# Optimization experiments

Measured on AMD Instinct MI355X. Metric: run time of the kernel, lower is better.

## Reference

```python
import jax, jax.numpy as jnp
import numpy as np

N_NODES = 50000
N_EDGES = 1600000
IN_C = 64
OUT_C = 64
N_CLASSES = 45


def setup_inputs() -> dict:
    key = jax.random.key(0)
    ks = jax.random.split(key, 12)

    def lin(k, i, o):
        return jax.random.normal(k, (i, o), jnp.float32) / np.float32(np.sqrt(i))

    return dict(
        x=jax.random.normal(ks[0], (N_NODES, IN_C), jnp.float32),
        edge_index=jax.random.randint(ks[1], (2, N_EDGES), 0, N_NODES, dtype=jnp.int32),
        W_z=lin(ks[2], IN_C, OUT_C), b_z=jnp.zeros((OUT_C,), jnp.float32),
        Wl_z=lin(ks[3], 2 * OUT_C, OUT_C), bl_z=jnp.zeros((OUT_C,), jnp.float32),
        W_r=lin(ks[4], IN_C, OUT_C), b_r=jnp.zeros((OUT_C,), jnp.float32),
        Wl_r=lin(ks[5], 2 * OUT_C, OUT_C), bl_r=jnp.zeros((OUT_C,), jnp.float32),
        W_h=lin(ks[6], IN_C, OUT_C), b_h=jnp.zeros((OUT_C,), jnp.float32),
        Wl_h=lin(ks[7], 2 * OUT_C, OUT_C), bl_h=jnp.zeros((OUT_C,), jnp.float32),
        W_out=lin(ks[8], OUT_C, N_CLASSES), b_out=jnp.zeros((N_CLASSES,), jnp.float32),
    )


def _gcn(x, W, b, src, dst, dinv):
    # GCNConv with improved self-loops (fill value 2.0):
    # out = D^{-1/2} (A + 2I) D^{-1/2} X W + b, with deg = in_degree + 2
    xw = x @ W                                   # [N, OUT_C]
    norm = dinv[src] * dinv[dst]                 # [E]
    agg = jax.ops.segment_sum(norm[:, None] * xw[src], dst, num_segments=N_NODES)
    agg = agg + (2.0 * dinv * dinv)[:, None] * xw  # self-loop contribution
    return agg + b


def reference(x, edge_index, W_z, b_z, Wl_z, bl_z, W_r, b_r, Wl_r, bl_r,
              W_h, b_h, Wl_h, bl_h, W_out, b_out):
    src, dst = edge_index[0], edge_index[1]
    deg = jax.ops.segment_sum(jnp.ones((N_EDGES,), jnp.float32), dst,
                              num_segments=N_NODES) + 2.0
    dinv = jax.lax.rsqrt(deg)

    # TGCN cell with H0 = 0 (no prior hidden state passed)
    H = jnp.zeros((N_NODES, OUT_C), x.dtype)
    Z = jax.nn.sigmoid(
        jnp.concatenate([_gcn(x, W_z, b_z, src, dst, dinv), H], axis=1) @ Wl_z + bl_z)
    R = jax.nn.sigmoid(
        jnp.concatenate([_gcn(x, W_r, b_r, src, dst, dinv), H], axis=1) @ Wl_r + bl_r)
    H_tilde = jnp.tanh(
        jnp.concatenate([_gcn(x, W_h, b_h, src, dst, dinv), H * R], axis=1) @ Wl_h + bl_h)
    H = Z * H + (1.0 - Z) * H_tilde

    # relu + linear readout to 45 classes
    return jax.nn.relu(H) @ W_out + b_out
```

## Files before the change

### kernel.cpp

```cpp
#include <hip/hip_runtime.h>

#define N_NODES 50000
#define N_EDGES 1600000
#define NB 782
#define NBB 256
#define CHUNK 6250
#define CAP 2560
#define SCAP 3072
#define ZROW 50000
#define NTILES 3125

typedef unsigned short ushort_t;
typedef _Float16 v8h __attribute__((ext_vector_type(8)));
typedef _Float16 v4h __attribute__((ext_vector_type(4)));
typedef float f32x4_t __attribute__((ext_vector_type(4)));

__global__ __launch_bounds__(256) void k_wprep(
    const float* __restrict__ Wz, const float* __restrict__ bz,
    const float* __restrict__ Wlz, const float* __restrict__ blz,
    const float* __restrict__ Wh, const float* __restrict__ bh,
    const float* __restrict__ Wlh, const float* __restrict__ blh,
    const float* __restrict__ Wout,
    float2* __restrict__ B2, _Float16* __restrict__ Bzh,
    _Float16* __restrict__ Bwo, int* __restrict__ gcur) {
  int t = blockIdx.x * 256 + threadIdx.x;
  {
    int lane = (t >> 3) & 63, j = t & 7;
    int ntile = t >> 10, ks = (t >> 9) & 1;
    int n = ntile * 16 + (lane & 15);
    int k = ks * 32 + ((lane >> 4) << 3) + j;
    float acc = 0.f;
    if (n < 64) {
      for (int q = 0; q < 64; ++q) acc = fmaf(Wz[k * 64 + q], Wlz[q * 64 + n], acc);
    } else {
      int n2 = n - 64;
      for (int q = 0; q < 64; ++q) acc = fmaf(Wh[k * 64 + q], Wlh[q * 64 + n2], acc);
    }
    Bzh[t] = (_Float16)acc;
  }
  if (t < 3072) {
    int lane = (t >> 3) & 63, j = t & 7;
    int ntile = t >> 10, ks = (t >> 9) & 1;
    int n = ntile * 16 + (lane & 15);
    int k = ks * 32 + ((lane >> 4) << 3) + j;
    Bwo[t] = (_Float16)((n < 45) ? Wout[k * 45 + n] : 0.f);
  }
  if (t < 64) {
    float vz = blz[t], vh = blh[t];
    for (int q = 0; q < 64; ++q) {
      vz = fmaf(bz[q], Wlz[q * 64 + t], vz);
      vh = fmaf(bh[q], Wlh[q * 64 + t], vh);
    }
    B2[t] = make_float2(vz, vh);
  }
  if (t < NB) gcur[t] = 0;
}

__global__ __launch_bounds__(256) void k_bin2(
    const int* __restrict__ ei, int* __restrict__ gcur, int* __restrict__ bins) {
  __shared__ int h[NB];
  __shared__ int segb[NB];
  __shared__ int pk[CHUNK];
  int tid = threadIdx.x, blk = blockIdx.x;
  for (int i = tid; i < NB; i += 256) h[i] = 0;
  __syncthreads();
  const int2* s2 = (const int2*)(ei + blk * CHUNK);
  const int2* d2 = (const int2*)(ei + N_EDGES + blk * CHUNK);
  for (int i = tid; i < CHUNK / 2; i += 256) {
    int2 s = s2[i];
    int2 d = d2[i];
    pk[2 * i]     = s.x | ((d.x & 63) << 16) | ((d.x >> 6) << 22);
    pk[2 * i + 1] = s.y | ((d.y & 63) << 16) | ((d.y >> 6) << 22);
    atomicAdd(&h[d.x >> 6], 1);
    atomicAdd(&h[d.y >> 6], 1);
  }
  __syncthreads();
  for (int b = tid; b < NB; b += 256) {
    int c = h[b];
    segb[b] = c ? atomicAdd(&gcur[b], c) : 0;
    h[b] = 0;
  }
  __syncthreads();
  for (int i = tid; i < CHUNK; i += 256) {
    int v = pk[i];
    int b = (unsigned)v >> 22;
    int p = atomicAdd(&h[b], 1);
    bins[b * CAP + segb[b] + p] = v & 0x3FFFFF;
  }
}

__global__ __launch_bounds__(256, 4) void k_sort(
    const int* __restrict__ bins, const int* __restrict__ gcur,
    const float* __restrict__ x,
    ushort_t* __restrict__ srcp, int2* __restrict__ rowiv,
    float* __restrict__ dinv, _Float16* __restrict__ xp) {
  __shared__ int dg[64], lo[64], cur[64];
  __shared__ float sdin[64];
  __shared__ int Tsh;
  __shared__ ushort_t buf[8192];
  int tid = threadIdx.x, b = blockIdx.x;
  int start = b * CAP, end = start + gcur[b];
  if (tid < 64) dg[tid] = 0;
  __syncthreads();
  for (int i = start + tid; i < end; i += 256)
    atomicAdd(&dg[bins[i] >> 16], 1);
  __syncthreads();
  int pdv = 0;
  if (tid < 64) { pdv = (dg[tid] + 7) & ~7; lo[tid] = pdv; }
  __syncthreads();
  for (int off = 1; off < 64; off <<= 1) {
    int u = 0;
    if (tid < 64 && tid >= off) u = lo[tid - off];
    __syncthreads();
    if (tid < 64) lo[tid] += u;
    __syncthreads();
  }
  int ex = 0;
  if (tid < 64) {
    ex = lo[tid] - pdv;
    cur[tid] = ex;
    if (tid == 63) Tsh = lo[63];
  }
  __syncthreads();
  int T = Tsh;
  int base = b * SCAP;
  for (int i = tid; i < T; i += 256) buf[i] = (ushort_t)ZROW;
  __syncthreads();
  for (int i = start + tid; i < end; i += 256) {
    int v = bins[i];
    int dl = v >> 16;
    int p = atomicAdd(&cur[dl], 1);
    buf[p] = (ushort_t)(v & 0xFFFF);
  }
  __syncthreads();
  for (int i = tid; i < T; i += 256) srcp[base + i] = buf[i];
  if (tid < 64) {
    int v = b * 64 + tid;
    if (v < N_NODES) {
      rowiv[v] = make_int2(base + ex, pdv);
      float dv = rsqrtf((float)dg[tid] + 2.0f);
      dinv[v] = dv;
      sdin[tid] = dv;
    } else {
      sdin[tid] = 0.f;
    }
  }
  __syncthreads();
  int nb64 = b * 4096;
  for (int idx = tid; idx < 4096; idx += 256) {
    int v = b * 64 + (idx >> 6);
    if (v < N_NODES) xp[nb64 + idx] = (_Float16)(sdin[idx >> 6] * x[nb64 + idx]);
  }
  if (b == 0 && tid < 64) xp[ZROW * 64 + tid] = (_Float16)0.f;
}

__global__ __launch_bounds__(256) void k_agg(
    const ushort_t* __restrict__ srcp, const int2* __restrict__ rowiv,
    const float* __restrict__ dinv, const _Float16* __restrict__ xp,
    _Float16* __restrict__ sxg) {
  int tid = threadIdx.x;
  int lane = tid & 63;
  int grp = lane >> 4;
  int sub = lane & 15;
  int chOff = sub << 2;
  int w = blockIdx.x * 4 + (tid >> 6);
  int nw = gridDim.x * 4;
  for (int v = w; v < N_NODES; v += nw) {
    int vu = __builtin_amdgcn_readfirstlane(v);
    int2 ri = rowiv[vu];
    int beg = ri.x, pd = ri.y;
    float aA0 = 0.f, aA1 = 0.f, aA2 = 0.f, aA3 = 0.f;
    float aB0 = 0.f, aB1 = 0.f, aB2 = 0.f, aB3 = 0.f;
    for (int e = beg; e < beg + pd; e += 64) {
      int rem = beg + pd - e;
      int m = rem < 64 ? rem : 64;
      int sv = (lane < m) ? (int)srcp[e + lane] : ZROW;
      for (int t = 0; t < m; t += 8) {
        int sA = __builtin_amdgcn_ds_bpermute((t + grp) << 2, sv);
        int sB = __builtin_amdgcn_ds_bpermute((t + 4 + grp) << 2, sv);
        v4h rA = *(const v4h*)(xp + (sA << 6) + chOff);
        v4h rB = *(const v4h*)(xp + (sB << 6) + chOff);
        aA0 += (float)rA[0]; aA1 += (float)rA[1];
        aA2 += (float)rA[2]; aA3 += (float)rA[3];
        aB0 += (float)rB[0]; aB1 += (float)rB[1];
        aB2 += (float)rB[2]; aB3 += (float)rB[3];
      }
    }
    float a0 = aA0 + aB0, a1 = aA1 + aB1, a2 = aA2 + aB2, a3 = aA3 + aB3;
    a0 += __shfl_xor(a0, 16); a1 += __shfl_xor(a1, 16);
    a2 += __shfl_xor(a2, 16); a3 += __shfl_xor(a3, 16);
    a0 += __shfl_xor(a0, 32); a1 += __shfl_xor(a1, 32);
    a2 += __shfl_xor(a2, 32); a3 += __shfl_xor(a3, 32);
    if (lane < 16) {
      float dv = dinv[vu];
      v4h self = *(const v4h*)(xp + (vu << 6) + chOff);
      v4h o;
      o[0] = (_Float16)(dv * a0 + 2.f * dv * (float)self[0]);
      o[1] = (_Float16)(dv * a1 + 2.f * dv * (float)self[1]);
      o[2] = (_Float16)(dv * a2 + 2.f * dv * (float)self[2]);
      o[3] = (_Float16)(dv * a3 + 2.f * dv * (float)self[3]);
      *(v4h*)(sxg + (vu << 6) + chOff) = o;
    }
  }
}

__global__ __launch_bounds__(256) void k_cell(
    const _Float16* __restrict__ sxg, const _Float16* __restrict__ Bzh,
    const _Float16* __restrict__ Bwo, const float2* __restrict__ B2,
    const float* __restrict__ bout, float* __restrict__ out) {
  __shared__ __align__(16) _Float16 tbuf[4][16][72];
  int tid = threadIdx.x;
  int lane = tid & 63, wv = tid >> 6;
  int l15 = lane & 15, quad = lane >> 4;
  int tile = blockIdx.x * 4 + wv;
  if (tile >= NTILES) return;

  v8h bzf[8][2], bwf[3][2];
  #pragma unroll
  for (int t = 0; t < 8; ++t)
    #pragma unroll
    for (int ks = 0; ks < 2; ++ks)
      bzf[t][ks] = *(const v8h*)(Bzh + (((t * 2 + ks) * 64 + lane) << 3));
  #pragma unroll
  for (int t = 0; t < 3; ++t)
    #pragma unroll
    for (int ks = 0; ks < 2; ++ks)
      bwf[t][ks] = *(const v8h*)(Bwo + (((t * 2 + ks) * 64 + lane) << 3));
  float zb[4], hb[4], ob[3];
  #pragma unroll
  for (int t = 0; t < 4; ++t) {
    float2 bb = B2[t * 16 + l15];
    zb[t] = bb.x; hb[t] = bb.y;
  }
  #pragma unroll
  for (int t = 0; t < 3; ++t) {
    int c = t * 16 + l15;
    ob[t] = (c < 45) ? bout[c] : 0.f;
  }

  const _Float16* ar = sxg + (tile * 16 + l15) * 64 + quad * 8;
  v8h a0 = *(const v8h*)ar;
  v8h a1 = *(const v8h*)(ar + 32);

  f32x4_t accz[8];
  #pragma unroll
  for (int t = 0; t < 8; ++t) {
    f32x4_t c4 = {0.f, 0.f, 0.f, 0.f};
    c4 = __builtin_amdgcn_mfma_f32_16x16x32_f16(a0, bzf[t][0], c4, 0, 0, 0);
    c4 = __builtin_amdgcn_mfma_f32_16x16x32_f16(a1, bzf[t][1], c4, 0, 0, 0);
    accz[t] = c4;
  }

  #pragma unroll
  for (int t = 0; t < 4; ++t) {
    #pragma unroll
    for (int r = 0; r < 4; ++r) {
      float zv = accz[t][r] + zb[t];
      float hv = accz[t + 4][r] + hb[t];
      float Z = 1.f / (1.f + __expf(-zv));
      float tt = fminf(15.f, fmaxf(-15.f, hv));
      float e2 = __expf(-2.f * tt);
      float Th = (1.f - e2) / (1.f + e2);
      tbuf[wv][quad * 4 + r][t * 16 + l15] = (_Float16)fmaxf((1.f - Z) * Th, 0.f);
    }
  }
  __asm__ volatile("s_waitcnt lgkmcnt(0)" ::: "memory");

  v8h p0 = *(const v8h*)&tbuf[wv][l15][quad * 8];
  v8h p1 = *(const v8h*)&tbuf[wv][l15][32 + quad * 8];

  #pragma unroll
  for (int t = 0; t < 3; ++t) {
    f32x4_t o4 = {0.f, 0.f, 0.f, 0.f};
    o4 = __builtin_amdgcn_mfma_f32_16x16x32_f16(p0, bwf[t][0], o4, 0, 0, 0);
    o4 = __builtin_amdgcn_mfma_f32_16x16x32_f16(p1, bwf[t][1], o4, 0, 0, 0);
    int c = t * 16 + l15;
    if (c < 45) {
      #pragma unroll
      for (int r = 0; r < 4; ++r)
        out[(tile * 16 + quad * 4 + r) * 45 + c] = o4[r] + ob[t];
    }
  }
}

extern "C" void kernel_launch(void* const* d_in, const int* in_sizes, int n_in,
                              void* d_out, int out_size, void* d_ws, size_t ws_size,
                              hipStream_t stream) {
  const float* x    = (const float*)d_in[0];
  const int*   ei   = (const int*)d_in[1];
  const float* Wz   = (const float*)d_in[2];
  const float* bz   = (const float*)d_in[3];
  const float* Wlz  = (const float*)d_in[4];
  const float* blz  = (const float*)d_in[5];
  const float* Wh   = (const float*)d_in[10];
  const float* bh   = (const float*)d_in[11];
  const float* Wlh  = (const float*)d_in[12];
  const float* blh  = (const float*)d_in[13];
  const float* Wout = (const float*)d_in[14];
  const float* bout = (const float*)d_in[15];
  float* out = (float*)d_out;

  char* w = (char*)d_ws;
  int*      bins  = (int*)(w + 0);
  _Float16* sxg   = (_Float16*)(w + 0);
  int*      gcur  = (int*)(w + 8007680);
  ushort_t* srcp  = (ushort_t*)(w + 8010816);
  int2*     rowiv = (int2*)(w + 12815424);
  float*    dinv  = (float*)(w + 13215424);
  float2*   B2    = (float2*)(w + 13415424);
  _Float16* Bzh   = (_Float16*)(w + 13415936);
  _Float16* Bwo   = (_Float16*)(w + 13432320);
  _Float16* xp    = (_Float16*)(w + 13438464);

  k_wprep<<<32, 256, 0, stream>>>(Wz, bz, Wlz, blz, Wh, bh, Wlh, blh, Wout,
                                  B2, Bzh, Bwo, gcur);
  k_bin2 <<<NBB, 256, 0, stream>>>(ei, gcur, bins);
  k_sort <<<NB, 256, 0, stream>>>(bins, gcur, x, srcp, rowiv, dinv, xp);
  k_agg  <<<2048, 256, 0, stream>>>(srcp, rowiv, dinv, xp, sxg);
  k_cell <<<NB, 256, 0, stream>>>(sxg, Bzh, Bwo, B2, bout, out);
}
```

Measured before the change: 166.3 us.

## Stage weight-fold GEMM in LDS, locally sort edge chunks, unroll gather loop

```diff
diff --git a/kernel.cpp b/kernel.cpp
--- a/kernel.cpp
+++ b/kernel.cpp
@@ -3,8 +3,8 @@
 #define N_NODES 50000
 #define N_EDGES 1600000
 #define NB 782
-#define NBB 256
-#define CHUNK 6250
+#define NBB 500
+#define CHUNK 3200
 #define CAP 2560
 #define SCAP 3072
 #define ZROW 50000
@@ -15,77 +15,124 @@
 typedef _Float16 v4h __attribute__((ext_vector_type(4)));
 typedef float f32x4_t __attribute__((ext_vector_type(4)));
 
-__global__ __launch_bounds__(256) void k_wprep(
+__global__ __launch_bounds__(256) void k_wprep2(
     const float* __restrict__ Wz, const float* __restrict__ bz,
     const float* __restrict__ Wlz, const float* __restrict__ blz,
     const float* __restrict__ Wh, const float* __restrict__ bh,
     const float* __restrict__ Wlh, const float* __restrict__ blh,
     const float* __restrict__ Wout,
-    float2* __restrict__ B2, _Float16* __restrict__ Bzh,
+    float* __restrict__ B2f, _Float16* __restrict__ Bzh,
     _Float16* __restrict__ Bwo, int* __restrict__ gcur) {
-  int t = blockIdx.x * 256 + threadIdx.x;
-  {
-    int lane = (t >> 3) & 63, j = t & 7;
-    int ntile = t >> 10, ks = (t >> 9) & 1;
-    int n = ntile * 16 + (lane & 15);
-    int k = ks * 32 + ((lane >> 4) << 3) + j;
-    float acc = 0.f;
-    if (n < 64) {
-      for (int q = 0; q < 64; ++q) acc = fmaf(Wz[k * 64 + q], Wlz[q * 64 + n], acc);
-    } else {
-      int n2 = n - 64;
-      for (int q = 0; q < 64; ++q) acc = fmaf(Wh[k * 64 + q], Wlh[q * 64 + n2], acc);
-    }
-    Bzh[t] = (_Float16)acc;
-  }
-  if (t < 3072) {
-    int lane = (t >> 3) & 63, j = t & 7;
-    int ntile = t >> 10, ks = (t >> 9) & 1;
-    int n = ntile * 16 + (lane & 15);
-    int k = ks * 32 + ((lane >> 4) << 3) + j;
-    Bwo[t] = (_Float16)((n < 45) ? Wout[k * 45 + n] : 0.f);
-  }
-  if (t < 64) {
-    float vz = blz[t], vh = blh[t];
-    for (int q = 0; q < 64; ++q) {
-      vz = fmaf(bz[q], Wlz[q * 64 + t], vz);
-      vh = fmaf(bh[q], Wlh[q * 64 + t], vh);
-    }
-    B2[t] = make_float2(vz, vh);
-  }
-  if (t < NB) gcur[t] = 0;
+  __shared__ float A[64 * 65];
+  __shared__ float Bm[64 * 65];
+  int tid = threadIdx.x, blk = blockIdx.x;
+  bool zpath = blk < 4;
+  if (blk == 2) {
+    for (int i = tid; i < NB; i += 256) gcur[i] = 0;
+  }
+  const float* Wsrc = zpath ? Wz : Wh;
+  const float* Lsrc = zpath ? Wlz : Wlh;
+  for (int idx = tid; idx < 4096; idx += 256) {
+    A[(idx >> 6) * 65 + (idx & 63)] = Wsrc[idx];
+    Bm[(idx >> 6) * 65 + (idx & 63)] = Lsrc[idx];
+  }
+  __syncthreads();
+
+  int lane = (tid >> 1) & 63;
+  int j0 = (tid & 1) * 4;
+  int ks = (tid >> 7) & 1;
+  int k0 = ks * 32 + ((lane >> 4) << 3) + j0;
+  int col = (blk & 3) * 16 + (lane & 15);
+  float a0 = 0.f, a1 = 0.f, a2 = 0.f, a3 = 0.f;
+  for (int q = 0; q < 64; ++q) {
+    float bv = Bm[q * 65 + col];
+    a0 = fmaf(A[k0 * 65 + q], bv, a0);
+    a1 = fmaf(A[(k0 + 1) * 65 + q], bv, a1);
+    a2 = fmaf(A[(k0 + 2) * 65 + q], bv, a2);
+    a3 = fmaf(A[(k0 + 3) * 65 + q], bv, a3);
+  }
+  int tb = blk * 1024 + tid * 4;
+  v4h o; o[0] = (_Float16)a0; o[1] = (_Float16)a1;
+  o[2] = (_Float16)a2; o[3] = (_Float16)a3;
+  *(v4h*)(Bzh + tb) = o;
+
+  if ((blk == 0 || blk == 4) && tid < 64) {
+    float v = zpath ? blz[tid] : blh[tid];
+    const float* bb = zpath ? bz : bh;
+    for (int q = 0; q < 64; ++q) v = fmaf(bb[q], Bm[q * 65 + tid], v);
+    B2f[tid * 2 + (zpath ? 0 : 1)] = v;
+  }
+  if (blk == 1) {
+    for (int e2 = 0; e2 < 12; ++e2) {
+      int t2 = tid * 12 + e2;
+      int ln = (t2 >> 3) & 63, j = t2 & 7;
+      int ntile = t2 >> 10, ks2 = (t2 >> 9) & 1;
+      int n = ntile * 16 + (ln & 15);
+      int k = ks2 * 32 + ((ln >> 4) << 3) + j;
+      Bwo[t2] = (_Float16)((n < 45) ? Wout[k * 45 + n] : 0.f);
+    }
+  }
 }
 
 __global__ __launch_bounds__(256) void k_bin2(
     const int* __restrict__ ei, int* __restrict__ gcur, int* __restrict__ bins) {
-  __shared__ int h[NB];
-  __shared__ int segb[NB];
-  __shared__ int pk[CHUNK];
+  __shared__ int h[NB], cur[NB], segb[NB];
+  __shared__ int ebuf[CHUNK];
+  __shared__ int scanT[256];
   int tid = threadIdx.x, blk = blockIdx.x;
   for (int i = tid; i < NB; i += 256) h[i] = 0;
   __syncthreads();
-  const int2* s2 = (const int2*)(ei + blk * CHUNK);
-  const int2* d2 = (const int2*)(ei + N_EDGES + blk * CHUNK);
+  int e0 = blk * CHUNK;
+  const int2* d2 = (const int2*)(ei + N_EDGES + e0);
+  for (int i = tid; i < CHUNK / 2; i += 256) {
+    int2 d = d2[i];
+    atomicAdd(&h[d.x >> 6], 1);
+    atomicAdd(&h[d.y >> 6], 1);
+  }
+  __syncthreads();
+  for (int b = tid; b < NB; b += 256) {
+    int c = h[b];
+    segb[b] = c ? atomicAdd(&gcur[b], c) : 0;
+  }
+  int vals[4], ts = 0;
+  #pragma unroll
+  for (int r = 0; r < 4; ++r) {
+    int idx = tid * 4 + r;
+    int v = (idx < NB) ? h[idx] : 0;
+    vals[r] = v; ts += v;
+  }
+  scanT[tid] = ts;
+  __syncthreads();
+  for (int off = 1; off < 256; off <<= 1) {
+    int u = (tid >= off) ? scanT[tid - off] : 0;
+    __syncthreads();
+    scanT[tid] += u;
+    __syncthreads();
+  }
+  int ex = scanT[tid] - ts;
+  #pragma unroll
+  for (int r = 0; r < 4; ++r) {
+    int idx = tid * 4 + r;
+    if (idx < NB) cur[idx] = ex;
+    ex += vals[r];
+  }
+  __syncthreads();
+  const int2* s2 = (const int2*)(ei + e0);
   for (int i = tid; i < CHUNK / 2; i += 256) {
     int2 s = s2[i];
     int2 d = d2[i];
-    pk[2 * i]     = s.x | ((d.x & 63) << 16) | ((d.x >> 6) << 22);
-    pk[2 * i + 1] = s.y | ((d.y & 63) << 16) | ((d.y >> 6) << 22);
-    atomicAdd(&h[d.x >> 6], 1);
-    atomicAdd(&h[d.y >> 6], 1);
-  }
-  __syncthreads();
-  for (int b = tid; b < NB; b += 256) {
-    int c = h[b];
-    segb[b] = c ? atomicAdd(&gcur[b], c) : 0;
-    h[b] = 0;
+    int b0 = d.x >> 6, b1 = d.y >> 6;
+    int p0 = atomicAdd(&cur[b0], 1);
+    ebuf[p0] = s.x | ((d.x & 63) << 16) | (b0 << 22);
+    int p1 = atomicAdd(&cur[b1], 1);
+    ebuf[p1] = s.y | ((d.y & 63) << 16) | (b1 << 22);
   }
   __syncthreads();
   for (int i = tid; i < CHUNK; i += 256) {
-    int v = pk[i];
+    int v = ebuf[i];
     int b = (unsigned)v >> 22;
-    int p = atomicAdd(&h[b], 1);
-    bins[b * CAP + segb[b] + p] = v & 0x3FFFFF;
+    int ex0 = cur[b] - h[b];
+    bins[b * CAP + segb[b] + (i - ex0)] = v & 0x3FFFFF;
   }
 }
 
@@ -97,7 +144,7 @@
   __shared__ int dg[64], lo[64], cur[64];
   __shared__ float sdin[64];
   __shared__ int Tsh;
-  __shared__ ushort_t buf[8192];
+  __shared__ ushort_t buf[3072];
   int tid = threadIdx.x, b = blockIdx.x;
   int start = b * CAP, end = start + gcur[b];
   if (tid < 64) dg[tid] = 0;
@@ -171,11 +218,32 @@
     int beg = ri.x, pd = ri.y;
     float aA0 = 0.f, aA1 = 0.f, aA2 = 0.f, aA3 = 0.f;
     float aB0 = 0.f, aB1 = 0.f, aB2 = 0.f, aB3 = 0.f;
+    float aC0 = 0.f, aC1 = 0.f, aC2 = 0.f, aC3 = 0.f;
+    float aD0 = 0.f, aD1 = 0.f, aD2 = 0.f, aD3 = 0.f;
     for (int e = beg; e < beg + pd; e += 64) {
       int rem = beg + pd - e;
       int m = rem < 64 ? rem : 64;
       int sv = (lane < m) ? (int)srcp[e + lane] : ZROW;
-      for (int t = 0; t < m; t += 8) {
+      int t = 0;
+      for (; t + 16 <= m; t += 16) {
+        int sA = __builtin_amdgcn_ds_bpermute((t + grp) << 2, sv);
+        int sB = __builtin_amdgcn_ds_bpermute((t + 4 + grp) << 2, sv);
+        int sC = __builtin_amdgcn_ds_bpermute((t + 8 + grp) << 2, sv);
+        int sD = __builtin_amdgcn_ds_bpermute((t + 12 + grp) << 2, sv);
+        v4h rA = *(const v4h*)(xp + (sA << 6) + chOff);
+        v4h rB = *(const v4h*)(xp + (sB << 6) + chOff);
+        v4h rC = *(const v4h*)(xp + (sC << 6) + chOff);
+        v4h rD = *(const v4h*)(xp + (sD << 6) + chOff);
+        aA0 += (float)rA[0]; aA1 += (float)rA[1];
+        aA2 += (float)rA[2]; aA3 += (float)rA[3];
+        aB0 += (float)rB[0]; aB1 += (float)rB[1];
+        aB2 += (float)rB[2]; aB3 += (float)rB[3];
+        aC0 += (float)rC[0]; aC1 += (float)rC[1];
+        aC2 += (float)rC[2]; aC3 += (float)rC[3];
+        aD0 += (float)rD[0]; aD1 += (float)rD[1];
+        aD2 += (float)rD[2]; aD3 += (float)rD[3];
+      }
+      if (t < m) {
         int sA = __builtin_amdgcn_ds_bpermute((t + grp) << 2, sv);
         int sB = __builtin_amdgcn_ds_bpermute((t + 4 + grp) << 2, sv);
         v4h rA = *(const v4h*)(xp + (sA << 6) + chOff);
@@ -186,7 +254,10 @@
         aB2 += (float)rB[2]; aB3 += (float)rB[3];
       }
     }
-    float a0 = aA0 + aB0, a1 = aA1 + aB1, a2 = aA2 + aB2, a3 = aA3 + aB3;
+    float a0 = (aA0 + aB0) + (aC0 + aD0);
+    float a1 = (aA1 + aB1) + (aC1 + aD1);
+    float a2 = (aA2 + aB2) + (aC2 + aD2);
+    float a3 = (aA3 + aB3) + (aC3 + aD3);
     a0 += __shfl_xor(a0, 16); a1 += __shfl_xor(a1, 16);
     a2 += __shfl_xor(a2, 16); a3 += __shfl_xor(a3, 16);
     a0 += __shfl_xor(a0, 32); a1 += __shfl_xor(a1, 32);
@@ -312,8 +383,8 @@
   _Float16* Bwo   = (_Float16*)(w + 13432320);
   _Float16* xp    = (_Float16*)(w + 13438464);
 
-  k_wprep<<<32, 256, 0, stream>>>(Wz, bz, Wlz, blz, Wh, bh, Wlh, blh, Wout,
-                                  B2, Bzh, Bwo, gcur);
+  k_wprep2<<<8, 256, 0, stream>>>(Wz, bz, Wlz, blz, Wh, bh, Wlh, blh, Wout,
+                                  (float*)B2, Bzh, Bwo, gcur);
   k_bin2 <<<NBB, 256, 0, stream>>>(ei, gcur, bins);
   k_sort <<<NB, 256, 0, stream>>>(bins, gcur, x, srcp, rowiv, dinv, xp);
   k_agg  <<<2048, 256, 0, stream>>>(srcp, rowiv, dinv, xp, sxg);
```

New measurement: 171.9 us. +3.4%, slower.
